# Performance work log

Measured on AMD Instinct MI355X. Metric: run time of the kernel, lower is better.

The kernel has to match this reference:

```python
import jax, jax.numpy as jnp
import numpy as np

NUM_NODES = 19
INPUT_DIM = 100
HIDDEN = 128
SEQ_LEN = 250
BATCH = 64
NUM_CLASSES = 4


def setup_inputs() -> dict:
    key = jax.random.key(0)
    ks = jax.random.split(key, 12)
    s_in = 1.0 / np.sqrt(HIDDEN)  # PyTorch LSTM init scale
    inputs = jax.random.normal(ks[0], (BATCH, NUM_NODES, SEQ_LEN, INPUT_DIM), dtype=jnp.float32)
    seq_lengths = jax.random.randint(ks[1], (BATCH,), 1, SEQ_LEN + 1, dtype=jnp.int64)
    # Per-node LSTM weights, PyTorch gate order (i, f, g, o) stacked on first axis.
    W_ih = jax.random.uniform(ks[2], (NUM_NODES, 4 * HIDDEN, INPUT_DIM), jnp.float32, -s_in, s_in)
    W_hh = jax.random.uniform(ks[3], (NUM_NODES, 4 * HIDDEN, HIDDEN), jnp.float32, -s_in, s_in)
    b_ih = jax.random.uniform(ks[4], (NUM_NODES, 4 * HIDDEN), jnp.float32, -s_in, s_in)
    b_hh = jax.random.uniform(ks[5], (NUM_NODES, 4 * HIDDEN), jnp.float32, -s_in, s_in)
    feat = NUM_NODES * HIDDEN
    s1 = 1.0 / np.sqrt(feat)
    s2 = 1.0 / np.sqrt(128)
    W1 = jax.random.uniform(ks[6], (128, feat), jnp.float32, -s1, s1)
    b1 = jax.random.uniform(ks[7], (128,), jnp.float32, -s1, s1)
    W2 = jax.random.uniform(ks[8], (NUM_CLASSES, 128), jnp.float32, -s2, s2)
    b2 = jax.random.uniform(ks[9], (NUM_CLASSES,), jnp.float32, -s2, s2)
    return {"inputs": inputs, "seq_lengths": seq_lengths,
            "W_ih": W_ih, "W_hh": W_hh, "b_ih": b_ih, "b_hh": b_hh,
            "W1": W1, "b1": b1, "W2": W2, "b2": b2}


def _grouped_lstm_last(inputs, W_ih, W_hh, b_ih, b_hh):
    # inputs: [B, N, T, D] -> last hidden state per node, [B, N, H]
    B, N, T, D = inputs.shape
    H = W_hh.shape[-1]
    x = jnp.transpose(inputs, (2, 1, 0, 3))  # [T, N, B, D]
    # Precompute input projections for all timesteps: [T, N, B, 4H]
    xg = jnp.einsum('tnbd,ngd->tnbg', x, W_ih) + (b_ih + b_hh)[None, :, None, :]

    def step(carry, xg_t):
        h, c = carry  # [N, B, H]
        gates = xg_t + jnp.einsum('nbh,ngh->nbg', h, W_hh)  # [N, B, 4H]
        i, f, g, o = jnp.split(gates, 4, axis=-1)  # PyTorch gate order i,f,g,o
        i = jax.nn.sigmoid(i)
        f = jax.nn.sigmoid(f)
        g = jnp.tanh(g)
        o = jax.nn.sigmoid(o)
        c = f * c + i * g
        h = o * jnp.tanh(c)
        return (h, c), None

    h0 = jnp.zeros((N, B, H), dtype=inputs.dtype)
    (h_last, _), _ = jax.lax.scan(step, (h0, h0), xg)
    return jnp.transpose(h_last, (1, 0, 2))  # [B, N, H]


def reference(inputs, seq_lengths, W_ih, W_hh, b_ih, b_hh, W1, b1, W2, b2):
    h = _grouped_lstm_last(inputs, W_ih, W_hh, b_ih, b_hh)  # [B, N, H]
    combined = h.reshape(h.shape[0], -1)  # concat over nodes -> [B, N*H]
    hidden = jax.nn.relu(combined @ W1.T + b1)  # dropout inactive (eval)
    return hidden @ W2.T + b2  # [B, num_classes]
```

## Files before the change

kernel.cpp:

```cpp
#include <hip/hip_runtime.h>
#include <hip/hip_bf16.h>

#define NN   19
#define DIN  100
#define HID  128
#define TT   250
#define BB   64
#define NC   4
#define FEAT 2432

typedef __attribute__((ext_vector_type(8))) short s8v;
typedef __attribute__((ext_vector_type(4))) float f4v;
typedef _Float16 h8v __attribute__((ext_vector_type(8)));
typedef _Float16 h4v __attribute__((ext_vector_type(4)));
typedef unsigned int u4v __attribute__((ext_vector_type(4)));

#define BFI_USH   1245184
#define V2_OFF_BFI  0ull
#define V2_OFF_BFH  2490368ull
#define V2_OFF_BIAS 4980736ull
#define V2_OFF_W1T  5019648ull
#define V2_OFF_HF   6264832ull
#define V2_NEED     6887424ull
#define PACK2_TOTAL (2*BFI_USH + 19*512 + FEAT*HID)

#define SZ_BF   (NN*8*4*8*512)
#define OFF_W1T_O (SZ_BF/2)
#define SZ_W1T  (FEAT*HID)
#define OFF_HF_O  (OFF_W1T_O + SZ_W1T)
#define PACK_TOTAL_O (SZ_BF + SZ_W1T)

#define RSTR 528

__device__ __forceinline__ unsigned short f2bf(float x) {
    union { float f; unsigned u; } v; v.f = x;
    unsigned r = v.u + 0x7FFF + ((v.u >> 16) & 1);
    return (unsigned short)(r >> 16);
}
#define LOG2E 1.4426950408889634f
__device__ __forceinline__ float sigf(float x) {
    return __builtin_amdgcn_rcpf(1.f + __builtin_amdgcn_exp2f(-LOG2E * x));
}
__device__ __forceinline__ float tnhf(float x) {
    return 1.f - 2.f * __builtin_amdgcn_rcpf(__builtin_amdgcn_exp2f(2.f * LOG2E * x) + 1.f);
}

__device__ __forceinline__ void pin8(h8v& v) {
    u4v u = __builtin_bit_cast(u4v, v);
    asm volatile("" : "+v"(u));
    v = __builtin_bit_cast(h8v, u);
}

__device__ __forceinline__ void lgkm_barrier() {
    asm volatile("s_waitcnt lgkmcnt(0)" ::: "memory");
    __builtin_amdgcn_s_barrier();
    asm volatile("" ::: "memory");
}


__global__ __launch_bounds__(256) void pack2_kernel(
        const float* __restrict__ W_ih, const float* __restrict__ W_hh,
        const float* __restrict__ b_ih, const float* __restrict__ b_hh,
        const float* __restrict__ W1, char* __restrict__ wsb) {
    int id = blockIdx.x * 256 + threadIdx.x;
    if (id < 2 * BFI_USH) {
        int which = id >= BFI_USH;
        int i = which ? id - BFI_USH : id;
        int e    = i & 7;
        int lane = (i >> 3) & 63;
        int kt   = (i >> 9) & 3;
        int nt   = (i >> 11) & 3;
        int hb   = (i >> 13) & 7;
        int n    = i >> 16;
        int k = kt * 32 + (lane >> 4) * 8 + e;
        int g = nt * 128 + hb * 16 + (lane & 15);
        float v;
        if (which) v = W_hh[((size_t)n * 512 + g) * HID + k];
        else       v = (k < DIN) ? W_ih[((size_t)n * 512 + g) * DIN + k] : 0.f;
        reinterpret_cast<_Float16*>(wsb)[id] = (_Float16)v;
        return;
    }
    int id2 = id - 2 * BFI_USH;
    if (id2 < NN * 512) {
        reinterpret_cast<float*>(wsb + V2_OFF_BIAS)[id2] = b_ih[id2] + b_hh[id2];
        return;
    }
    int id3 = id2 - NN * 512;
    if (id3 < FEAT * HID) {
        int j = id3 & 127, k = id3 >> 7;
        reinterpret_cast<float*>(wsb + V2_OFF_W1T)[id3] = W1[(size_t)j * FEAT + k];
    }
}

__global__ __launch_bounds__(512, 2) void lstm8c_kernel(
        const char* __restrict__ wsb, const float* __restrict__ inp,
        float* __restrict__ hf) {
    __shared__ alignas(16) _Float16 xh[2][16 * 264];

    const int tid  = threadIdx.x;
    const int lane = tid & 63;
    const int w8   = tid >> 6;
    const int l15  = lane & 15;
    const int g4   = lane >> 4;
    const int n    = blockIdx.x >> 3;
    const int oct  = blockIdx.x & 7;
    const int bq   = oct >> 1;
    const int hi   = oct & 1;
    const int hb   = w8;
    const int j    = hb * 16 + l15;

    h8v bf[4][4], bfx[4][4];
    {
        const _Float16* wph = reinterpret_cast<const _Float16*>(wsb + V2_OFF_BFH)
                              + (size_t)lane * 8;
        const _Float16* wpx = reinterpret_cast<const _Float16*>(wsb + V2_OFF_BFI)
                              + (size_t)lane * 8;
        #pragma unroll
        for (int nt = 0; nt < 4; ++nt)
            #pragma unroll
            for (int kt = 0; kt < 4; ++kt) {
                size_t off = ((size_t)((n * 8 + hb) * 16 + nt * 4 + kt)) * 512;
                bf[nt][kt]  = *reinterpret_cast<const h8v*>(wph + off);
                bfx[nt][kt] = *reinterpret_cast<const h8v*>(wpx + off);
            }
        #pragma unroll
        for (int nt = 0; nt < 4; ++nt)
            #pragma unroll
            for (int kt = 0; kt < 4; ++kt) {
                pin8(bf[nt][kt]);
                pin8(bfx[nt][kt]);
            }
    }
    float bs[4];
    #pragma unroll
    for (int nt = 0; nt < 4; ++nt)
        bs[nt] = reinterpret_cast<const float*>(wsb + V2_OFF_BIAS)[n * 512 + nt * 128 + j];

    for (int i = tid; i < 2 * 16 * 264; i += 512) (&xh[0][0])[i] = (_Float16)0.f;

    const bool st = tid < 200;
    const int sr  = st ? tid / 25 : 0;
    const int c4  = st ? tid - sr * 25 : 0;
    const int g4s = sr >> 1, qs = sr & 1;
    const int tr  = g4s * 4 + qs;
    const int Rr  = (g4s & 1) * 4 + (g4s >> 1) * 2 + qs;
    const float* xb = inp + (size_t)((bq * 16 + hi * 8 + Rr) * NN + n) * (TT * DIN)
                      + c4 * 4;
    const int wofs_x = tr * RSTR + c4 * 8;

    const int arow = l15 * RSTR;
    const int wr0 = (g4 * 4) * RSTR + 256 + 2 * j;
    const int wr1 = (g4 * 4 + 1) * RSTR + 256 + 2 * j;

    float c2[2] = {0.f, 0.f};
    float h2[2] = {0.f, 0.f};

    __syncthreads();
    if (st) {
        float4 v = *reinterpret_cast<const float4*>(xb);
        h4v pk = {(_Float16)v.x, (_Float16)v.y, (_Float16)v.z, (_Float16)v.w};
        *reinterpret_cast<h4v*>(reinterpret_cast<char*>(xh[0]) + wofs_x) = pk;
    }
    __syncthreads();

    #pragma unroll 2
    for (int t = 0; t < TT; ++t) {
        char* rc = reinterpret_cast<char*>(xh[t & 1]);
        char* wc = reinterpret_cast<char*>(xh[(t + 1) & 1]);

        float4 nxt = make_float4(0.f, 0.f, 0.f, 0.f);
        if (t < TT - 1 && st)
            nxt = *reinterpret_cast<const float4*>(xb + (t + 1) * DIN);

        f4v acc[4];
        #pragma unroll
        for (int nt = 0; nt < 4; ++nt)
            acc[nt] = (f4v){bs[nt], bs[nt], 0.f, 0.f};

        h8v ax0 = *reinterpret_cast<const h8v*>(rc + arow + (0 * 64 + g4 * 16));
        h8v ax1 = *reinterpret_cast<const h8v*>(rc + arow + (1 * 64 + g4 * 16));
        h8v ax2 = *reinterpret_cast<const h8v*>(rc + arow + (2 * 64 + g4 * 16));
        h8v ax3 = *reinterpret_cast<const h8v*>(rc + arow + (3 * 64 + g4 * 16));
        #pragma unroll
        for (int nt = 0; nt < 4; ++nt) {
            acc[nt] = __builtin_amdgcn_mfma_f32_16x16x32_f16(ax0, bfx[nt][0], acc[nt], 0, 0, 0);
            acc[nt] = __builtin_amdgcn_mfma_f32_16x16x32_f16(ax1, bfx[nt][1], acc[nt], 0, 0, 0);
            acc[nt] = __builtin_amdgcn_mfma_f32_16x16x32_f16(ax2, bfx[nt][2], acc[nt], 0, 0, 0);
            acc[nt] = __builtin_amdgcn_mfma_f32_16x16x32_f16(ax3, bfx[nt][3], acc[nt], 0, 0, 0);
        }

        h8v ah0 = *reinterpret_cast<const h8v*>(rc + arow + (256 + 0 * 64 + g4 * 16));
        h8v ah1 = *reinterpret_cast<const h8v*>(rc + arow + (256 + 1 * 64 + g4 * 16));
        h8v ah2 = *reinterpret_cast<const h8v*>(rc + arow + (256 + 2 * 64 + g4 * 16));
        h8v ah3 = *reinterpret_cast<const h8v*>(rc + arow + (256 + 3 * 64 + g4 * 16));

        acc[0] = __builtin_amdgcn_mfma_f32_16x16x32_f16(ah0, bf[0][0], acc[0], 0, 0, 0);
        acc[0] = __builtin_amdgcn_mfma_f32_16x16x32_f16(ah1, bf[0][1], acc[0], 0, 0, 0);
        acc[0] = __builtin_amdgcn_mfma_f32_16x16x32_f16(ah2, bf[0][2], acc[0], 0, 0, 0);
        acc[0] = __builtin_amdgcn_mfma_f32_16x16x32_f16(ah3, bf[0][3], acc[0], 0, 0, 0);
        float ii0 = sigf(acc[0][0]);
        float ii1 = sigf(acc[0][1]);

        acc[1] = __builtin_amdgcn_mfma_f32_16x16x32_f16(ah0, bf[1][0], acc[1], 0, 0, 0);
        acc[1] = __builtin_amdgcn_mfma_f32_16x16x32_f16(ah1, bf[1][1], acc[1], 0, 0, 0);
        acc[1] = __builtin_amdgcn_mfma_f32_16x16x32_f16(ah2, bf[1][2], acc[1], 0, 0, 0);
        acc[1] = __builtin_amdgcn_mfma_f32_16x16x32_f16(ah3, bf[1][3], acc[1], 0, 0, 0);
        float ff0 = sigf(acc[1][0]);
        float ff1 = sigf(acc[1][1]);

        acc[2] = __builtin_amdgcn_mfma_f32_16x16x32_f16(ah0, bf[2][0], acc[2], 0, 0, 0);
        acc[2] = __builtin_amdgcn_mfma_f32_16x16x32_f16(ah1, bf[2][1], acc[2], 0, 0, 0);
        acc[2] = __builtin_amdgcn_mfma_f32_16x16x32_f16(ah2, bf[2][2], acc[2], 0, 0, 0);
        acc[2] = __builtin_amdgcn_mfma_f32_16x16x32_f16(ah3, bf[2][3], acc[2], 0, 0, 0);
        float gg0 = tnhf(acc[2][0]);
        float gg1 = tnhf(acc[2][1]);

        acc[3] = __builtin_amdgcn_mfma_f32_16x16x32_f16(ah0, bf[3][0], acc[3], 0, 0, 0);
        acc[3] = __builtin_amdgcn_mfma_f32_16x16x32_f16(ah1, bf[3][1], acc[3], 0, 0, 0);
        acc[3] = __builtin_amdgcn_mfma_f32_16x16x32_f16(ah2, bf[3][2], acc[3], 0, 0, 0);
        acc[3] = __builtin_amdgcn_mfma_f32_16x16x32_f16(ah3, bf[3][3], acc[3], 0, 0, 0);
        float oo0 = sigf(acc[3][0]);
        float oo1 = sigf(acc[3][1]);

        float cn0 = ff0 * c2[0] + ii0 * gg0;
        c2[0] = cn0;
        float hn0 = oo0 * tnhf(cn0);
        h2[0] = hn0;
        *reinterpret_cast<_Float16*>(wc + wr0) = (_Float16)hn0;

        float cn1 = ff1 * c2[1] + ii1 * gg1;
        c2[1] = cn1;
        float hn1 = oo1 * tnhf(cn1);
        h2[1] = hn1;
        *reinterpret_cast<_Float16*>(wc + wr1) = (_Float16)hn1;

        if (t < TT - 1 && st) {
            h4v pk = {(_Float16)nxt.x, (_Float16)nxt.y, (_Float16)nxt.z, (_Float16)nxt.w};
            *reinterpret_cast<h4v*>(wc + wofs_x) = pk;
        }
        lgkm_barrier();
    }

    #pragma unroll
    for (int q = 0; q < 2; ++q) {
        int b = bq * 16 + hi * 8 + (g4 & 1) * 4 + (g4 >> 1) * 2 + q;
        hf[((size_t)b * NN + n) * HID + j] = h2[q];
    }
}

__global__ __launch_bounds__(256) void head2_kernel(
        const float* __restrict__ hf, const float* __restrict__ w1t,
        const float* __restrict__ b1, const float* __restrict__ W2,
        const float* __restrict__ b2, float* __restrict__ out) {
    __shared__ float comb[FEAT];
    __shared__ float par[2][HID];
    __shared__ float hid[HID];
    const int b = blockIdx.x;
    const int u  = threadIdx.x & 127;
    const int kk = threadIdx.x >> 7;
    const float* hfp = hf + (size_t)b * FEAT;
    for (int i = threadIdx.x; i < FEAT; i += 256) comb[i] = hfp[i];
    __syncthreads();

    const int k0 = kk * (FEAT / 2);
    float acc = 0.f;
    #pragma unroll 8
    for (int k = 0; k < FEAT / 2; ++k)
        acc = fmaf(comb[k0 + k], w1t[(size_t)(k0 + k) * HID + u], acc);
    par[kk][u] = acc;
    __syncthreads();
    if (kk == 0) hid[u] = fmaxf(par[0][u] + par[1][u] + b1[u], 0.f);
    __syncthreads();

    if (threadIdx.x < NC) {
        int cls = threadIdx.x;
        float a = b2[cls];
        #pragma unroll 4
        for (int k = 0; k < HID; ++k)
            a = fmaf(hid[k], W2[cls * HID + k], a);
        out[b * NC + cls] = a;
    }
}

__global__ __launch_bounds__(256) void packfb_kernel(
        const float* __restrict__ W_ih, const float* __restrict__ W_hh,
        const float* __restrict__ W1,
        unsigned short* __restrict__ bfw, float* __restrict__ w1t) {
    int id = blockIdx.x * 256 + threadIdx.x;
    if (id < SZ_BF) {
        int e    = id & 7;
        int lane = (id >> 3) & 63;
        int kt   = (id >> 9) & 7;
        int nt   = (id >> 12) & 3;
        int hb   = (id >> 14) & 7;
        int n    = id >> 17;
        int k = kt * 32 + (lane >> 4) * 8 + e;
        int g = nt * 128 + hb * 16 + (lane & 15);
        float v = 0.f;
        if (k < DIN)       v = W_ih[((size_t)n * 512 + g) * DIN + k];
        else if (k < 228)  v = W_hh[((size_t)n * 512 + g) * HID + (k - DIN)];
        bfw[id] = f2bf(v);
        return;
    }
    int id3 = id - SZ_BF;
    if (id3 < SZ_W1T) {
        int j = id3 & 127, k = id3 >> 7;
        w1t[id3] = W1[(size_t)j * FEAT + k];
    }
}

__global__ __launch_bounds__(512, 2) void lstmfb_kernel(
        const float* __restrict__ inp,
        const float* __restrict__ b_ih, const float* __restrict__ b_hh,
        const unsigned short* __restrict__ bfw, float* __restrict__ hf) {
    __shared__ alignas(16) unsigned short xh[2][16 * 256];
    const int tid  = threadIdx.x;
    const int lane = tid & 63;
    const int w    = tid >> 6;
    const int l15  = lane & 15;
    const int g4   = lane >> 4;
    const int n    = blockIdx.x >> 2;
    const int bq   = blockIdx.x & 3;
    const int j    = w * 16 + l15;

    s8v bf[4][8];
    const unsigned short* wp = bfw + ((size_t)(n * 8 + w) * 32) * 512 + lane * 8;
    #pragma unroll
    for (int nt = 0; nt < 4; ++nt)
        #pragma unroll
        for (int kt = 0; kt < 8; ++kt)
            bf[nt][kt] = *reinterpret_cast<const s8v*>(wp + (nt * 8 + kt) * 512);

    float bs[4];
    #pragma unroll
    for (int nt = 0; nt < 4; ++nt)
        bs[nt] = b_ih[n * 512 + nt * 128 + j] + b_hh[n * 512 + nt * 128 + j];

    float c[4] = {0.f, 0.f, 0.f, 0.f};
    float h[4] = {0.f, 0.f, 0.f, 0.f};
    for (int i = tid; i < 2 * 16 * 256; i += 512) (&xh[0][0])[i] = 0;

    const bool st = tid < 400;
    const int row = st ? tid / 25 : 0;
    const int c4  = st ? tid - row * 25 : 0;
    const float* xb = inp + ((size_t)(bq * 16 + row) * NN + n) * (TT * DIN) + c4 * 4;
    const int wofs = row * 512 + ((c4 * 8) ^ ((row & 7) << 4));
    const int arow = l15 * 512;
    const int aswz = (l15 & 7) << 4;

    __syncthreads();
    if (st) {
        float4 v = *reinterpret_cast<const float4*>(xb);
        unsigned lo = f2bf(v.x) | ((unsigned)f2bf(v.y) << 16);
        unsigned hi = f2bf(v.z) | ((unsigned)f2bf(v.w) << 16);
        *reinterpret_cast<uint2*>(reinterpret_cast<char*>(xh[0]) + wofs) =
            make_uint2(lo, hi);
    }
    __syncthreads();

    for (int t = 0; t < TT; ++t) {
        char* rc = reinterpret_cast<char*>(xh[t & 1]);
        char* wc = reinterpret_cast<char*>(xh[(t + 1) & 1]);
        float4 nxt = make_float4(0.f, 0.f, 0.f, 0.f);
        if (t < TT - 1 && st)
            nxt = *reinterpret_cast<const float4*>(xb + (t + 1) * DIN);

        f4v acc[4];
        #pragma unroll
        for (int nt = 0; nt < 4; ++nt)
            acc[nt] = (f4v){bs[nt], bs[nt], bs[nt], bs[nt]};
        #pragma unroll
        for (int kt = 0; kt < 8; ++kt) {
            s8v a = *reinterpret_cast<const s8v*>(rc + arow + ((kt * 64 + g4 * 16) ^ aswz));
            #pragma unroll
            for (int nt = 0; nt < 4; ++nt)
                acc[nt] = __builtin_amdgcn_mfma_f32_16x16x32_bf16(a, bf[nt][kt], acc[nt], 0, 0, 0);
        }
        #pragma unroll
        for (int r = 0; r < 4; ++r) {
            float ii = sigf(acc[0][r]);
            float ff = sigf(acc[1][r]);
            float gg = tnhf(acc[2][r]);
            float oo = sigf(acc[3][r]);
            float cn = ff * c[r] + ii * gg;
            c[r] = cn;
            float hn = oo * tnhf(cn);
            h[r] = hn;
            int rr = g4 * 4 + r;
            *reinterpret_cast<unsigned short*>(
                wc + rr * 512 + (((DIN + j) * 2) ^ ((rr & 7) << 4))) = f2bf(hn);
        }
        if (t < TT - 1 && st) {
            unsigned lo = f2bf(nxt.x) | ((unsigned)f2bf(nxt.y) << 16);
            unsigned hi = f2bf(nxt.z) | ((unsigned)f2bf(nxt.w) << 16);
            *reinterpret_cast<uint2*>(wc + wofs) = make_uint2(lo, hi);
        }
        __syncthreads();
    }
    #pragma unroll
    for (int r = 0; r < 4; ++r) {
        int b = bq * 16 + g4 * 4 + r;
        hf[((size_t)b * NN + n) * HID + j] = h[r];
    }
}

extern "C" void kernel_launch(void* const* d_in, const int* in_sizes, int n_in,
                              void* d_out, int out_size, void* d_ws, size_t ws_size,
                              hipStream_t stream) {
    const float* inp  = (const float*)d_in[0];
    const float* W_ih = (const float*)d_in[2];
    const float* W_hh = (const float*)d_in[3];
    const float* b_ih = (const float*)d_in[4];
    const float* b_hh = (const float*)d_in[5];
    const float* W1   = (const float*)d_in[6];
    const float* b1   = (const float*)d_in[7];
    const float* W2   = (const float*)d_in[8];
    const float* b2   = (const float*)d_in[9];
    float* out = (float*)d_out;

    if (ws_size >= V2_NEED) {
        char* wsb = (char*)d_ws;
        float* hf  = (float*)(wsb + V2_OFF_HF);
        float* w1t = (float*)(wsb + V2_OFF_W1T);
        pack2_kernel<<<(PACK2_TOTAL + 255) / 256, 256, 0, stream>>>(
            W_ih, W_hh, b_ih, b_hh, W1, wsb);
        lstm8c_kernel<<<NN * 8, 512, 0, stream>>>(wsb, inp, hf);
        head2_kernel<<<BB, 256, 0, stream>>>(hf, w1t, b1, W2, b2, out);
    } else {
        float* ws = (float*)d_ws;
        unsigned short* bfw = (unsigned short*)d_ws;
        packfb_kernel<<<(PACK_TOTAL_O + 255) / 256, 256, 0, stream>>>(
            W_ih, W_hh, W1, bfw, ws + OFF_W1T_O);
        lstmfb_kernel<<<NN * 4, 512, 0, stream>>>(inp, b_ih, b_hh, bfw, ws + OFF_HF_O);
        head2_kernel<<<BB, 256, 0, stream>>>(ws + OFF_HF_O, ws + OFF_W1T_O,
                                             b1, W2, b2, out);
    }
}
```

Before: 283.5 us.

## Batch input projection for two timesteps per iteration using unused MFMA rows

The LSTM loop now handles two timesteps per iteration. The input-projection MFMAs fill all four accumulator rows, covering timesteps t and t+1, and the second half is carried in registers. This halves the x-projection MFMA work and the x-tile loads per timestep by using output rows that were previously padding. The hidden state gets its own double buffer and there are two barriers per pair of steps. The x staging now uses 400 threads and clamps the prefetch index at the end.

```diff
diff --git a/kernel.cpp b/kernel.cpp
--- a/kernel.cpp
+++ b/kernel.cpp
@@ -30,7 +30,7 @@
 #define OFF_HF_O  (OFF_W1T_O + SZ_W1T)
 #define PACK_TOTAL_O (SZ_BF + SZ_W1T)
 
-#define RSTR 528
+#define XSTR 272
 
 __device__ __forceinline__ unsigned short f2bf(float x) {
     union { float f; unsigned u; } v; v.f = x;
@@ -92,10 +92,11 @@
     }
 }
 
-__global__ __launch_bounds__(512, 2) void lstm8c_kernel(
+__global__ __launch_bounds__(512, 2) void lstm9p_kernel(
         const char* __restrict__ wsb, const float* __restrict__ inp,
         float* __restrict__ hf) {
-    __shared__ alignas(16) _Float16 xh[2][16 * 264];
+    __shared__ alignas(16) _Float16 xt[2][16 * 136];
+    __shared__ alignas(16) _Float16 ht[2][16 * 136];
 
     const int tid  = threadIdx.x;
     const int lane = tid & 63;
@@ -136,51 +137,60 @@
     for (int nt = 0; nt < 4; ++nt)
         bs[nt] = reinterpret_cast<const float*>(wsb + V2_OFF_BIAS)[n * 512 + nt * 128 + j];
 
-    for (int i = tid; i < 2 * 16 * 264; i += 512) (&xh[0][0])[i] = (_Float16)0.f;
-
-    const bool st = tid < 200;
+    for (int i = tid; i < 16 * 136; i += 512) {
+        xt[0][i] = (_Float16)0.f; xt[1][i] = (_Float16)0.f;
+        ht[0][i] = (_Float16)0.f; ht[1][i] = (_Float16)0.f;
+    }
+
+    const bool st = tid < 400;
     const int sr  = st ? tid / 25 : 0;
-    const int c4  = st ? tid - sr * 25 : 0;
-    const int g4s = sr >> 1, qs = sr & 1;
-    const int tr  = g4s * 4 + qs;
-    const int Rr  = (g4s & 1) * 4 + (g4s >> 1) * 2 + qs;
-    const float* xb = inp + (size_t)((bq * 16 + hi * 8 + Rr) * NN + n) * (TT * DIN)
-                      + c4 * 4;
-    const int wofs_x = tr * RSTR + c4 * 8;
-
-    const int arow = l15 * RSTR;
-    const int wr0 = (g4 * 4) * RSTR + 256 + 2 * j;
-    const int wr1 = (g4 * 4 + 1) * RSTR + 256 + 2 * j;
+    const int d4  = st ? tid - sr * 25 : 0;
+    const int g4s = sr >> 2, qs = sr & 3;
+    const int tpo = qs >> 1;
+    const int Rr  = (g4s & 1) * 4 + (g4s >> 1) * 2 + (qs & 1);
+    const float* xbp = inp + (size_t)((bq * 16 + hi * 8 + Rr) * NN + n) * (TT * DIN)
+                       + d4 * 4;
+    const int wofs_x = sr * XSTR + d4 * 8;
+
+    const int arow = l15 * XSTR;
+    const int wr0 = (g4 * 4) * XSTR + 2 * j;
+    const int wr1 = (g4 * 4 + 1) * XSTR + 2 * j;
 
     float c2[2] = {0.f, 0.f};
     float h2[2] = {0.f, 0.f};
 
     __syncthreads();
     if (st) {
-        float4 v = *reinterpret_cast<const float4*>(xb);
+        float4 v = *reinterpret_cast<const float4*>(xbp + (size_t)tpo * DIN);
         h4v pk = {(_Float16)v.x, (_Float16)v.y, (_Float16)v.z, (_Float16)v.w};
-        *reinterpret_cast<h4v*>(reinterpret_cast<char*>(xh[0]) + wofs_x) = pk;
-    }
-    __syncthreads();
-
-    #pragma unroll 2
-    for (int t = 0; t < TT; ++t) {
-        char* rc = reinterpret_cast<char*>(xh[t & 1]);
-        char* wc = reinterpret_cast<char*>(xh[(t + 1) & 1]);
+        *reinterpret_cast<h4v*>(reinterpret_cast<char*>(xt[0]) + wofs_x) = pk;
+    }
+    __syncthreads();
+
+    float pend[8];
+
+    for (int tp = 0; tp < 125; ++tp) {
+        const char* rx = reinterpret_cast<const char*>(xt[tp & 1]);
+        char*       wx = reinterpret_cast<char*>(xt[(tp + 1) & 1]);
+        const char* rh0 = reinterpret_cast<const char*>(ht[0]);
+        char*       wh1 = reinterpret_cast<char*>(ht[1]);
 
         float4 nxt = make_float4(0.f, 0.f, 0.f, 0.f);
-        if (t < TT - 1 && st)
-            nxt = *reinterpret_cast<const float4*>(xb + (t + 1) * DIN);
+        if (st) {
+            int tl = 2 * tp + 2 + tpo;
+            if (tl > 249) tl = 249;
+            nxt = *reinterpret_cast<const float4*>(xbp + (size_t)tl * DIN);
+        }
 
         f4v acc[4];
         #pragma unroll
         for (int nt = 0; nt < 4; ++nt)
-            acc[nt] = (f4v){bs[nt], bs[nt], 0.f, 0.f};
-
-        h8v ax0 = *reinterpret_cast<const h8v*>(rc + arow + (0 * 64 + g4 * 16));
-        h8v ax1 = *reinterpret_cast<const h8v*>(rc + arow + (1 * 64 + g4 * 16));
-        h8v ax2 = *reinterpret_cast<const h8v*>(rc + arow + (2 * 64 + g4 * 16));
-        h8v ax3 = *reinterpret_cast<const h8v*>(rc + arow + (3 * 64 + g4 * 16));
+            acc[nt] = (f4v){bs[nt], bs[nt], bs[nt], bs[nt]};
+
+        h8v ax0 = *reinterpret_cast<const h8v*>(rx + arow + (0 * 64 + g4 * 16));
+        h8v ax1 = *reinterpret_cast<const h8v*>(rx + arow + (1 * 64 + g4 * 16));
+        h8v ax2 = *reinterpret_cast<const h8v*>(rx + arow + (2 * 64 + g4 * 16));
+        h8v ax3 = *reinterpret_cast<const h8v*>(rx + arow + (3 * 64 + g4 * 16));
         #pragma unroll
         for (int nt = 0; nt < 4; ++nt) {
             acc[nt] = __builtin_amdgcn_mfma_f32_16x16x32_f16(ax0, bfx[nt][0], acc[nt], 0, 0, 0);
@@ -189,10 +199,10 @@
             acc[nt] = __builtin_amdgcn_mfma_f32_16x16x32_f16(ax3, bfx[nt][3], acc[nt], 0, 0, 0);
         }
 
-        h8v ah0 = *reinterpret_cast<const h8v*>(rc + arow + (256 + 0 * 64 + g4 * 16));
-        h8v ah1 = *reinterpret_cast<const h8v*>(rc + arow + (256 + 1 * 64 + g4 * 16));
-        h8v ah2 = *reinterpret_cast<const h8v*>(rc + arow + (256 + 2 * 64 + g4 * 16));
-        h8v ah3 = *reinterpret_cast<const h8v*>(rc + arow + (256 + 3 * 64 + g4 * 16));
+        h8v ah0 = *reinterpret_cast<const h8v*>(rh0 + arow + (0 * 64 + g4 * 16));
+        h8v ah1 = *reinterpret_cast<const h8v*>(rh0 + arow + (1 * 64 + g4 * 16));
+        h8v ah2 = *reinterpret_cast<const h8v*>(rh0 + arow + (2 * 64 + g4 * 16));
+        h8v ah3 = *reinterpret_cast<const h8v*>(rh0 + arow + (3 * 64 + g4 * 16));
 
         acc[0] = __builtin_amdgcn_mfma_f32_16x16x32_f16(ah0, bf[0][0], acc[0], 0, 0, 0);
         acc[0] = __builtin_amdgcn_mfma_f32_16x16x32_f16(ah1, bf[0][1], acc[0], 0, 0, 0);
@@ -222,22 +232,81 @@
         float oo0 = sigf(acc[3][0]);
         float oo1 = sigf(acc[3][1]);
 
+        #pragma unroll
+        for (int nt = 0; nt < 4; ++nt) {
+            pend[nt * 2]     = acc[nt][2];
+            pend[nt * 2 + 1] = acc[nt][3];
+        }
+
         float cn0 = ff0 * c2[0] + ii0 * gg0;
         c2[0] = cn0;
         float hn0 = oo0 * tnhf(cn0);
         h2[0] = hn0;
-        *reinterpret_cast<_Float16*>(wc + wr0) = (_Float16)hn0;
+        *reinterpret_cast<_Float16*>(wh1 + wr0) = (_Float16)hn0;
 
         float cn1 = ff1 * c2[1] + ii1 * gg1;
         c2[1] = cn1;
         float hn1 = oo1 * tnhf(cn1);
         h2[1] = hn1;
-        *reinterpret_cast<_Float16*>(wc + wr1) = (_Float16)hn1;
-
-        if (t < TT - 1 && st) {
+        *reinterpret_cast<_Float16*>(wh1 + wr1) = (_Float16)hn1;
+
+        if (st) {
             h4v pk = {(_Float16)nxt.x, (_Float16)nxt.y, (_Float16)nxt.z, (_Float16)nxt.w};
-            *reinterpret_cast<h4v*>(wc + wofs_x) = pk;
-        }
+            *reinterpret_cast<h4v*>(wx + wofs_x) = pk;
+        }
+        lgkm_barrier();
+
+        #pragma unroll
+        for (int nt = 0; nt < 4; ++nt)
+            acc[nt] = (f4v){pend[nt * 2], pend[nt * 2 + 1], 0.f, 0.f};
+
+        const char* rh1 = reinterpret_cast<const char*>(ht[1]);
+        char*       wh0 = reinterpret_cast<char*>(ht[0]);
+        h8v bh0 = *reinterpret_cast<const h8v*>(rh1 + arow + (0 * 64 + g4 * 16));
+        h8v bh1 = *reinterpret_cast<const h8v*>(rh1 + arow + (1 * 64 + g4 * 16));
+        h8v bh2 = *reinterpret_cast<const h8v*>(rh1 + arow + (2 * 64 + g4 * 16));
+        h8v bh3 = *reinterpret_cast<const h8v*>(rh1 + arow + (3 * 64 + g4 * 16));
+
+        acc[0] = __builtin_amdgcn_mfma_f32_16x16x32_f16(bh0, bf[0][0], acc[0], 0, 0, 0);
+        acc[0] = __builtin_amdgcn_mfma_f32_16x16x32_f16(bh1, bf[0][1], acc[0], 0, 0, 0);
+        acc[0] = __builtin_amdgcn_mfma_f32_16x16x32_f16(bh2, bf[0][2], acc[0], 0, 0, 0);
+        acc[0] = __builtin_amdgcn_mfma_f32_16x16x32_f16(bh3, bf[0][3], acc[0], 0, 0, 0);
+        float jj0 = sigf(acc[0][0]);
+        float jj1 = sigf(acc[0][1]);
+
+        acc[1] = __builtin_amdgcn_mfma_f32_16x16x32_f16(bh0, bf[1][0], acc[1], 0, 0, 0);
+        acc[1] = __builtin_amdgcn_mfma_f32_16x16x32_f16(bh1, bf[1][1], acc[1], 0, 0, 0);
+        acc[1] = __builtin_amdgcn_mfma_f32_16x16x32_f16(bh2, bf[1][2], acc[1], 0, 0, 0);
+        acc[1] = __builtin_amdgcn_mfma_f32_16x16x32_f16(bh3, bf[1][3], acc[1], 0, 0, 0);
+        float kk0 = sigf(acc[1][0]);
+        float kk1 = sigf(acc[1][1]);
+
+        acc[2] = __builtin_amdgcn_mfma_f32_16x16x32_f16(bh0, bf[2][0], acc[2], 0, 0, 0);
+        acc[2] = __builtin_amdgcn_mfma_f32_16x16x32_f16(bh1, bf[2][1], acc[2], 0, 0, 0);
+        acc[2] = __builtin_amdgcn_mfma_f32_16x16x32_f16(bh2, bf[2][2], acc[2], 0, 0, 0);
+        acc[2] = __builtin_amdgcn_mfma_f32_16x16x32_f16(bh3, bf[2][3], acc[2], 0, 0, 0);
+        float ll0 = tnhf(acc[2][0]);
+        float ll1 = tnhf(acc[2][1]);
+
+        acc[3] = __builtin_amdgcn_mfma_f32_16x16x32_f16(bh0, bf[3][0], acc[3], 0, 0, 0);
+        acc[3] = __builtin_amdgcn_mfma_f32_16x16x32_f16(bh1, bf[3][1], acc[3], 0, 0, 0);
+        acc[3] = __builtin_amdgcn_mfma_f32_16x16x32_f16(bh2, bf[3][2], acc[3], 0, 0, 0);
+        acc[3] = __builtin_amdgcn_mfma_f32_16x16x32_f16(bh3, bf[3][3], acc[3], 0, 0, 0);
+        float mm0 = sigf(acc[3][0]);
+        float mm1 = sigf(acc[3][1]);
+
+        float dn0 = kk0 * c2[0] + jj0 * ll0;
+        c2[0] = dn0;
+        float gn0 = mm0 * tnhf(dn0);
+        h2[0] = gn0;
+        *reinterpret_cast<_Float16*>(wh0 + wr0) = (_Float16)gn0;
+
+        float dn1 = kk1 * c2[1] + jj1 * ll1;
+        c2[1] = dn1;
+        float gn1 = mm1 * tnhf(dn1);
+        h2[1] = gn1;
+        *reinterpret_cast<_Float16*>(wh0 + wr1) = (_Float16)gn1;
+
         lgkm_barrier();
     }
 
@@ -424,7 +493,7 @@
         float* w1t = (float*)(wsb + V2_OFF_W1T);
         pack2_kernel<<<(PACK2_TOTAL + 255) / 256, 256, 0, stream>>>(
             W_ih, W_hh, b_ih, b_hh, W1, wsb);
-        lstm8c_kernel<<<NN * 8, 512, 0, stream>>>(wsb, inp, hf);
+        lstm9p_kernel<<<NN * 8, 512, 0, stream>>>(wsb, inp, hf);
         head2_kernel<<<BB, 256, 0, stream>>>(hf, w1t, b1, W2, b2, out);
     } else {
         float* ws = (float*)d_ws;
```

Result: faster. 277.8 us (-2.0%).
